# Kernel optimization log

Measured on AMD Instinct MI355X. Metric: run time of the kernel, lower is better.

## Reference

```python
import jax, jax.numpy as jnp
import numpy as np

B, T, C = 4, 2048, 768
N_HEADS = 16
HEAD_DIM = C // N_HEADS  # 48
ROPE_BASE = 10000.0


def setup_inputs() -> dict:
    key = jax.random.key(0)
    ks = jax.random.split(key, 6)
    s = 0.02
    return {
        "hidden_states": jax.random.normal(ks[0], (B, T, C), dtype=jnp.float32),
        "attention_mask": jnp.ones((B, T), dtype=jnp.float32),
        "Wq": jax.random.normal(ks[1], (C, C), dtype=jnp.float32) * s,
        "bq": jnp.zeros((C,), dtype=jnp.float32),
        "Wk": jax.random.normal(ks[2], (C, C), dtype=jnp.float32) * s,
        "bk": jnp.zeros((C,), dtype=jnp.float32),
        "Wv": jax.random.normal(ks[3], (C, C), dtype=jnp.float32) * s,
        "bv": jnp.zeros((C,), dtype=jnp.float32),
        "Wo": jax.random.normal(ks[4], (C, C), dtype=jnp.float32) * s,
        "bo": jnp.zeros((C,), dtype=jnp.float32),
    }


def _rotate_half(x):
    x1, x2 = jnp.split(x, 2, axis=-1)
    return jnp.concatenate([-x2, x1], axis=-1)


def reference(hidden_states, attention_mask, Wq, bq, Wk, bk, Wv, bv, Wo, bo):
    b, t, c = hidden_states.shape
    h, d = N_HEADS, c // N_HEADS

    def split_heads(x):  # [b,t,c] -> [b,h,t,d]
        return x.reshape(b, t, h, d).transpose(0, 2, 1, 3)

    q = split_heads(hidden_states @ Wq.T + bq)
    k = split_heads(hidden_states @ Wk.T + bk)
    v = split_heads(hidden_states @ Wv.T + bv)

    # rotary embedding: cos/sin [t, d]
    pos = jnp.arange(t, dtype=jnp.float32)
    inv_freq = 1.0 / (ROPE_BASE ** (jnp.arange(0, d, 2, dtype=jnp.float32) / d))
    freqs = pos[:, None] * inv_freq[None, :]          # [t, d/2]
    emb = jnp.concatenate([freqs, freqs], axis=-1)    # [t, d]
    cos, sin = jnp.cos(emb), jnp.sin(emb)
    q = q * cos + _rotate_half(q) * sin
    k = k * cos + _rotate_half(k) * sin

    scores = jnp.einsum('bhqd,bhkd->bhqk', q, k) / jnp.sqrt(jnp.asarray(d, q.dtype))
    # additive padding mask: (1 - mask) * -10000, broadcast [b,1,1,t]
    scores = scores + (1.0 - attention_mask)[:, None, None, :] * -10000.0
    # causal mask with -inf
    causal = jnp.tril(jnp.ones((t, t), dtype=bool))
    scores = jnp.where(causal[None, None], scores, -jnp.inf)

    probs = jax.nn.softmax(scores, axis=-1)
    ctx = jnp.einsum('bhqk,bhkd->bhqd', probs, v)
    ctx = ctx.transpose(0, 2, 1, 3).reshape(b, t, c)
    return ctx @ Wo.T + bo
```

## Files before the change

kernel.cpp:

```cpp
#include <hip/hip_runtime.h>
#include <hip/hip_bf16.h>
#include <math.h>

#define BB 4
#define TT 2048
#define CC 768
#define NHD 16
#define HD 48
#define NQT 32

typedef __hip_bfloat16 bf16;
typedef __attribute__((ext_vector_type(8))) short short8;
typedef __attribute__((ext_vector_type(4))) float floatx4;

__device__ __forceinline__ unsigned short f2bf(float x) {
    bf16 h = __float2bfloat16(x);
    return *(unsigned short*)&h;
}
__device__ __forceinline__ float bfu2f(unsigned short u) {
    return __uint_as_float(((unsigned)u) << 16);
}

__device__ __forceinline__ void gl_lds16(const void* g, void* s) {
    __builtin_amdgcn_global_load_lds((const __attribute__((address_space(1))) void*)g,
                                     (__attribute__((address_space(3))) void*)s, 16, 0, 0);
}

__global__ __launch_bounds__(256) void cast_hs(const float* __restrict__ src,
                                               unsigned short* __restrict__ dst) {
    int i = (blockIdx.x * 256 + threadIdx.x) * 4;
    float4 v = *(const float4*)(src + i);
    ushort4 p;
    p.x = f2bf(v.x); p.y = f2bf(v.y); p.z = f2bf(v.z); p.w = f2bf(v.w);
    *(ushort4*)(dst + i) = p;
}

__global__ __launch_bounds__(256) void cast_w4(const float* __restrict__ s0, const float* __restrict__ s1,
                                               const float* __restrict__ s2, const float* __restrict__ s3,
                                               unsigned short* __restrict__ d0, unsigned short* __restrict__ d1,
                                               unsigned short* __restrict__ d2, unsigned short* __restrict__ d3) {
    const float* s; unsigned short* d;
    switch (blockIdx.y) {
        case 0: s = s0; d = d0; break;
        case 1: s = s1; d = d1; break;
        case 2: s = s2; d = d2; break;
        default: s = s3; d = d3; break;
    }
    int i = (blockIdx.x * 256 + threadIdx.x) * 4;
    float4 v = *(const float4*)(s + i);
    ushort4 p;
    p.x = f2bf(v.x); p.y = f2bf(v.y); p.z = f2bf(v.z); p.w = f2bf(v.w);
    *(ushort4*)(d + i) = p;
}

template <int MODE>
__global__ __launch_bounds__(256) void gemm_mfma(const unsigned short* __restrict__ A,
                                                 const unsigned short* __restrict__ Bw,
                                                 const float* __restrict__ b0p,
                                                 const float* __restrict__ b1p,
                                                 const float* __restrict__ b2p,
                                                 void* __restrict__ out0,
                                                 void* __restrict__ out1,
                                                 void* __restrict__ out2) {
    __shared__ __align__(16) unsigned short As[128][32];
    __shared__ __align__(16) unsigned short Bs[128][32];
    const int tid = threadIdx.x;
    const int w = tid >> 6, lane = tid & 63;
    const int quad = lane >> 4, ln = lane & 15;
    const int wr = w >> 1, wc = w & 1;
    const int n0 = blockIdx.x * 128;
    const int m0 = blockIdx.y * 128;

    const int srow = lane >> 2, sseg = lane & 3;
    const unsigned short* agp0 = A + (size_t)(m0 + w * 16 + srow) * CC + sseg * 8;
    const unsigned short* agp1 = A + (size_t)(m0 + 64 + w * 16 + srow) * CC + sseg * 8;
    const unsigned short* bgp0 = Bw + (size_t)(n0 + w * 16 + srow) * CC + sseg * 8;
    const unsigned short* bgp1 = Bw + (size_t)(n0 + 64 + w * 16 + srow) * CC + sseg * 8;
    void* asl0 = &As[w * 16][0];
    void* asl1 = &As[64 + w * 16][0];
    void* bsl0 = &Bs[w * 16][0];
    void* bsl1 = &Bs[64 + w * 16][0];

    floatx4 acc[4][4];
#pragma unroll
    for (int mi = 0; mi < 4; ++mi)
#pragma unroll
        for (int ni = 0; ni < 4; ++ni) acc[mi][ni] = (floatx4){0.f, 0.f, 0.f, 0.f};

    for (int k0 = 0; k0 < CC; k0 += 32) {
        __syncthreads();
        gl_lds16(agp0 + k0, asl0);
        gl_lds16(agp1 + k0, asl1);
        gl_lds16(bgp0 + k0, bsl0);
        gl_lds16(bgp1 + k0, bsl1);
        __syncthreads();
        short8 af[4], bfr[4];
#pragma unroll
        for (int mi = 0; mi < 4; ++mi) af[mi] = *(const short8*)&As[wr * 64 + mi * 16 + ln][quad * 8];
#pragma unroll
        for (int ni = 0; ni < 4; ++ni) bfr[ni] = *(const short8*)&Bs[wc * 64 + ni * 16 + ln][quad * 8];
#pragma unroll
        for (int mi = 0; mi < 4; ++mi)
#pragma unroll
            for (int ni = 0; ni < 4; ++ni)
                acc[mi][ni] = __builtin_amdgcn_mfma_f32_16x16x32_bf16(af[mi], bfr[ni], acc[mi][ni], 0, 0, 0);
    }

    if (MODE == 0) {
        float* outf = (float*)out0;
        float bv[4];
#pragma unroll
        for (int ni = 0; ni < 4; ++ni) bv[ni] = b0p[n0 + wc * 64 + ni * 16 + ln];
#pragma unroll
        for (int mi = 0; mi < 4; ++mi)
#pragma unroll
            for (int r = 0; r < 4; ++r) {
                size_t row = m0 + wr * 64 + mi * 16 + quad * 4 + r;
#pragma unroll
                for (int ni = 0; ni < 4; ++ni)
                    outf[row * CC + n0 + wc * 64 + ni * 16 + ln] = acc[mi][ni][r] + bv[ni];
            }
    } else {
        const int seg = n0 / CC;
        const int nl0 = n0 - seg * CC;
        const float* bp = (seg == 0) ? b0p : (seg == 1) ? b1p : b2p;
        float bv[4];
#pragma unroll
        for (int ni = 0; ni < 4; ++ni) bv[ni] = bp[nl0 + wc * 64 + ni * 16 + ln];

        if (seg < 2) {
            unsigned short* outb = (unsigned short*)(seg == 0 ? out0 : out1);
#pragma unroll
            for (int mi = 0; mi < 4; ++mi)
#pragma unroll
                for (int r = 0; r < 4; ++r) {
                    size_t row = m0 + wr * 64 + mi * 16 + quad * 4 + r;
#pragma unroll
                    for (int ni = 0; ni < 4; ++ni)
                        outb[row * CC + nl0 + wc * 64 + ni * 16 + ln] = f2bf(acc[mi][ni][r] + bv[ni]);
                }
        } else {
            unsigned short* outb = (unsigned short*)out2;
            const int b = m0 >> 11;
#pragma unroll
            for (int ni = 0; ni < 4; ++ni) {
                int col = nl0 + wc * 64 + ni * 16 + ln;
                int h = col / HD, d = col % HD;
                size_t base = (size_t)((b * NHD + h) * HD + d) * TT;
#pragma unroll
                for (int mi = 0; mi < 4; ++mi) {
                    int t = (m0 & 2047) + wr * 64 + mi * 16 + quad * 4;
                    ushort4 pk;
                    pk.x = f2bf(acc[mi][ni][0] + bv[ni]);
                    pk.y = f2bf(acc[mi][ni][1] + bv[ni]);
                    pk.z = f2bf(acc[mi][ni][2] + bv[ni]);
                    pk.w = f2bf(acc[mi][ni][3] + bv[ni]);
                    *(ushort4*)(outb + base + t) = pk;
                }
            }
        }
    }
}

__global__ __launch_bounds__(256) void rope_bf(unsigned short* __restrict__ q,
                                               unsigned short* __restrict__ k) {
    int idx = blockIdx.x * blockDim.x + threadIdx.x;
    const int HALF = HD / 2;
    int p = idx % HALF;
    int rest = idx / HALF;
    int h = rest % NHD;
    int n = rest / NHD;
    int t = n % TT;
    float inv_freq = powf(10000.0f, -((float)(2 * p) / (float)HD));
    float ang = (float)t * inv_freq;
    float sn, cs;
    sincosf(ang, &sn, &cs);
    size_t base = (size_t)n * CC + h * HD + p;
    float x1 = bfu2f(q[base]), x2 = bfu2f(q[base + HALF]);
    q[base] = f2bf(x1 * cs - x2 * sn);
    q[base + HALF] = f2bf(x2 * cs + x1 * sn);
    x1 = bfu2f(k[base]); x2 = bfu2f(k[base + HALF]);
    k[base] = f2bf(x1 * cs - x2 * sn);
    k[base + HALF] = f2bf(x2 * cs + x1 * sn);
}

__global__ __launch_bounds__(256) void attn_kernel(const unsigned short* __restrict__ qb,
                                                   const unsigned short* __restrict__ kb,
                                                   const unsigned short* __restrict__ vt,
                                                   const float* __restrict__ amask,
                                                   unsigned short* __restrict__ ctx) {
    const int pair = blockIdx.x, h = blockIdx.y, b = blockIdx.z;
    const int tid = threadIdx.x;
    const int w = tid >> 6, lane = tid & 63;
    const int g = lane >> 4, ln = lane & 15;

    __shared__ __align__(16) unsigned short Qs[64][72];
    __shared__ __align__(16) unsigned short Ks[64][72];
    __shared__ __align__(16) unsigned short Vs[48][72];
    __shared__ __align__(16) unsigned short Pw[4][16][72];
    __shared__ __align__(16) float Mb[64];
    __shared__ __align__(16) float alpha_s[4][16];
    __shared__ __align__(16) float l_s[4][16];

    {
        short8 z8 = {0, 0, 0, 0, 0, 0, 0, 0};
        if (tid < 128) {
            *(short8*)&Qs[tid >> 1][48 + (tid & 1) * 8] = z8;
        } else {
            int t2 = tid - 128;
            *(short8*)&Ks[t2 >> 1][48 + (t2 & 1) * 8] = z8;
        }
    }

    const int ck1 = tid + 256;
    const int rK0 = tid / 6, sK0 = tid % 6;
    const int rK1 = ck1 / 6, sK1 = ck1 % 6;
    const int rV0 = tid >> 3, sV0 = tid & 7;
    const int rV1 = ck1 >> 3, sV1 = ck1 & 7;
    const unsigned short* kbase0 = kb + (size_t)(b * TT + rK0) * CC + h * HD + sK0 * 8;
    const unsigned short* kbase1 = kb + (size_t)(b * TT + rK1) * CC + h * HD + sK1 * 8;
    const unsigned short* vbase0 = vt + (size_t)((b * NHD + h) * HD + rV0) * TT + sV0 * 8;
    const unsigned short* vbase1 = vt + (size_t)((b * NHD + h) * HD + rV1) * TT + sV1 * 8;
    const float* mbase = amask + b * TT + (tid & 63);

    const float scale = 0.14433756729740643f;

    for (int rep = 0; rep < 2; ++rep) {
        const int qt = rep ? (NQT - 1 - pair) : pair;
        const int q0 = qt * 64;
        __syncthreads();
        *(short8*)&Qs[rK0][sK0 * 8] =
            *(const short8*)(qb + (size_t)(b * TT + q0 + rK0) * CC + h * HD + sK0 * 8);
        if (tid < 128)
            *(short8*)&Qs[rK1][sK1 * 8] =
                *(const short8*)(qb + (size_t)(b * TT + q0 + rK1) * CC + h * HD + sK1 * 8);

        const unsigned short* kp0 = kbase0;
        const unsigned short* kp1 = kbase1;
        const unsigned short* vp0 = vbase0;
        const unsigned short* vp1 = vbase1;
        const float* mp = mbase;
        short8 kr0, kr1, vr0, vr1;
        float mr = 1.0f;
        kr0 = *(const short8*)kp0;
        vr0 = *(const short8*)vp0;
        if (tid < 128) { kr1 = *(const short8*)kp1; vr1 = *(const short8*)vp1; }
        if (tid < 64) mr = *mp;
        __syncthreads();

        short8 aq0 = *(const short8*)&Qs[w * 16 + ln][g * 8];
        short8 aq1 = *(const short8*)&Qs[w * 16 + ln][32 + g * 8];
        const int q_lane = q0 + w * 16 + ln;

        float m_i = -1e30f, l_i = 0.f;
        floatx4 o0 = {0.f, 0.f, 0.f, 0.f}, o1 = o0, o2 = o0;

        for (int kt = 0; kt <= qt; ++kt) {
            __syncthreads();
            *(short8*)&Ks[rK0][sK0 * 8] = kr0;
            *(short8*)&Vs[rV0][sV0 * 8] = vr0;
            if (tid < 128) {
                *(short8*)&Ks[rK1][sK1 * 8] = kr1;
                *(short8*)&Vs[rV1][sV1 * 8] = vr1;
            }
            if (tid < 64) Mb[tid] = (1.0f - mr) * -10000.0f;
            __syncthreads();

            if (kt < qt) {
                kp0 += (size_t)64 * CC; kr0 = *(const short8*)kp0;
                vp0 += 64;              vr0 = *(const short8*)vp0;
                if (tid < 128) {
                    kp1 += (size_t)64 * CC; kr1 = *(const short8*)kp1;
                    vp1 += 64;              vr1 = *(const short8*)vp1;
                }
                if (tid < 64) { mp += 64; mr = *mp; }
            }

            const int k0 = kt * 64;
            floatx4 sc[4];
#pragma unroll
            for (int c = 0; c < 4; ++c) {
                short8 kf0 = *(const short8*)&Ks[c * 16 + ln][g * 8];
                short8 kf1 = *(const short8*)&Ks[c * 16 + ln][32 + g * 8];
                floatx4 z = {0.f, 0.f, 0.f, 0.f};
                z = __builtin_amdgcn_mfma_f32_16x16x32_bf16(kf0, aq0, z, 0, 0, 0);
                z = __builtin_amdgcn_mfma_f32_16x16x32_bf16(kf1, aq1, z, 0, 0, 0);
                sc[c] = z;
            }

            const bool diag = (kt == qt);
            float p[4][4];
            float mloc = -1e30f;
#pragma unroll
            for (int c = 0; c < 4; ++c) {
                floatx4 mb4 = *(const floatx4*)&Mb[c * 16 + g * 4];
#pragma unroll
                for (int r = 0; r < 4; ++r) {
                    float s = sc[c][r] * scale + mb4[r];
                    if (diag && (k0 + c * 16 + g * 4 + r > q_lane)) s = -1e30f;
                    p[c][r] = s;
                    mloc = fmaxf(mloc, s);
                }
            }
            mloc = fmaxf(mloc, __shfl_xor(mloc, 16));
            mloc = fmaxf(mloc, __shfl_xor(mloc, 32));
            float mnew = fmaxf(m_i, mloc);
            float alpha = __expf(m_i - mnew);
            float rs = 0.f;
#pragma unroll
            for (int c = 0; c < 4; ++c)
#pragma unroll
                for (int r = 0; r < 4; ++r) {
                    float pv = __expf(p[c][r] - mnew);
                    p[c][r] = pv;
                    rs += pv;
                }
            rs += __shfl_xor(rs, 16);
            rs += __shfl_xor(rs, 32);
            m_i = mnew;
            l_i = l_i * alpha + rs;

            if (g == 0) alpha_s[w][ln] = alpha;
            floatx4 a4 = *(const floatx4*)&alpha_s[w][g * 4];
#pragma unroll
            for (int r = 0; r < 4; ++r) { o0[r] *= a4[r]; o1[r] *= a4[r]; o2[r] *= a4[r]; }

#pragma unroll
            for (int c = 0; c < 4; ++c) {
                ushort4 pk;
                pk.x = f2bf(p[c][0]); pk.y = f2bf(p[c][1]);
                pk.z = f2bf(p[c][2]); pk.w = f2bf(p[c][3]);
                *(ushort4*)&Pw[w][ln][c * 16 + g * 4] = pk;
            }
            short8 pa0 = *(const short8*)&Pw[w][ln][g * 8];
            short8 pa1 = *(const short8*)&Pw[w][ln][32 + g * 8];
#pragma unroll
            for (int n = 0; n < 3; ++n) {
                short8 vb0 = *(const short8*)&Vs[n * 16 + ln][g * 8];
                short8 vb1 = *(const short8*)&Vs[n * 16 + ln][32 + g * 8];
                floatx4 acc = (n == 0) ? o0 : (n == 1) ? o1 : o2;
                acc = __builtin_amdgcn_mfma_f32_16x16x32_bf16(pa0, vb0, acc, 0, 0, 0);
                acc = __builtin_amdgcn_mfma_f32_16x16x32_bf16(pa1, vb1, acc, 0, 0, 0);
                if (n == 0) o0 = acc; else if (n == 1) o1 = acc; else o2 = acc;
            }
        }

        if (g == 0) l_s[w][ln] = l_i;
        floatx4 l4 = *(const floatx4*)&l_s[w][g * 4];
#pragma unroll
        for (int r = 0; r < 4; ++r) {
            float inv_l = 1.0f / l4[r];
            int t = q0 + w * 16 + g * 4 + r;
            unsigned short* dst = ctx + (size_t)(b * TT + t) * CC + h * HD;
            dst[ln] = f2bf(o0[r] * inv_l);
            dst[16 + ln] = f2bf(o1[r] * inv_l);
            dst[32 + ln] = f2bf(o2[r] * inv_l);
        }
    }
}

extern "C" void kernel_launch(void* const* d_in, const int* in_sizes, int n_in,
                              void* d_out, int out_size, void* d_ws, size_t ws_size,
                              hipStream_t stream) {
    const float* hs = (const float*)d_in[0];
    const float* amask = (const float*)d_in[1];
    const float* Wq = (const float*)d_in[2];
    const float* bq = (const float*)d_in[3];
    const float* Wk = (const float*)d_in[4];
    const float* bk = (const float*)d_in[5];
    const float* Wv = (const float*)d_in[6];
    const float* bv = (const float*)d_in[7];
    const float* Wo = (const float*)d_in[8];
    const float* bo = (const float*)d_in[9];

    const size_t NELEM = (size_t)BB * TT * CC;
    const size_t WELEM = (size_t)CC * CC;
    unsigned short* hb  = (unsigned short*)d_ws;
    unsigned short* qbuf = hb + NELEM;
    unsigned short* kbuf = qbuf + NELEM;
    unsigned short* vtb = kbuf + NELEM;
    unsigned short* ctxb = vtb + NELEM;
    unsigned short* wqb = ctxb + NELEM;
    unsigned short* wkb = wqb + WELEM;
    unsigned short* wvb = wkb + WELEM;
    unsigned short* wob = wvb + WELEM;

    cast_hs<<<NELEM / 1024, 256, 0, stream>>>(hs, hb);
    dim3 wgrid(WELEM / 1024, 4);
    cast_w4<<<wgrid, 256, 0, stream>>>(Wq, Wk, Wv, Wo, wqb, wkb, wvb, wob);

    dim3 qkvgrid(3 * CC / 128, (BB * TT) / 128);
    gemm_mfma<1><<<qkvgrid, 256, 0, stream>>>(hb, wqb, bq, bk, bv, qbuf, kbuf, vtb);

    int rope_total = BB * TT * NHD * (HD / 2);
    rope_bf<<<rope_total / 256, 256, 0, stream>>>(qbuf, kbuf);

    dim3 agrid(NQT / 2, NHD, BB);
    attn_kernel<<<agrid, 256, 0, stream>>>(qbuf, kbuf, vtb, amask, ctxb);

    dim3 ogrid(CC / 128, (BB * TT) / 128);
    gemm_mfma<0><<<ogrid, 256, 0, stream>>>(ctxb, wob, bo, nullptr, nullptr,
                                            (float*)d_out, nullptr, nullptr);
}
```

Baseline: 271.5 us.

## Widen GEMM K-tile with swizzled LDS, fold softmax scale and mask into QK MFMA

The projection GEMM now stages 64-wide K tiles with an XOR-swizzled shared-memory layout, halving the number of barrier pairs and avoiding LDS bank conflicts. The softmax scale and log2(e) are folded into Q during RoPE. The padding mask bias is stored as an extra K column, matched by a 1.0 in Q's padding lane, so the MFMA adds it directly. Softmax switches to exp2, and probabilities are packed to bf16 with a cheap round-half-up bit trick instead of the full conversion. This trades a small precision change (bf16-rounded mask bias and Q scale, non-RNE rounding) for fewer ALU ops in the attention inner loop.

```diff
diff --git a/kernel.cpp b/kernel.cpp
--- a/kernel.cpp
+++ b/kernel.cpp
@@ -24,6 +24,12 @@
 __device__ __forceinline__ void gl_lds16(const void* g, void* s) {
     __builtin_amdgcn_global_load_lds((const __attribute__((address_space(1))) void*)g,
                                      (__attribute__((address_space(3))) void*)s, 16, 0, 0);
+}
+
+__device__ __forceinline__ unsigned int pk_bf2(float a, float b) {
+    unsigned int ua = __float_as_uint(a) + 0x8000u;
+    unsigned int ub = __float_as_uint(b) + 0x8000u;
+    return __builtin_amdgcn_perm(ub, ua, 0x07060302);
 }
 
 __global__ __launch_bounds__(256) void cast_hs(const float* __restrict__ src,
@@ -62,8 +68,8 @@
                                                  void* __restrict__ out0,
                                                  void* __restrict__ out1,
                                                  void* __restrict__ out2) {
-    __shared__ __align__(16) unsigned short As[128][32];
-    __shared__ __align__(16) unsigned short Bs[128][32];
+    __shared__ __align__(16) unsigned short As[128][64];
+    __shared__ __align__(16) unsigned short Bs[128][64];
     const int tid = threadIdx.x;
     const int w = tid >> 6, lane = tid & 63;
     const int quad = lane >> 4, ln = lane & 15;
@@ -71,15 +77,20 @@
     const int n0 = blockIdx.x * 128;
     const int m0 = blockIdx.y * 128;
 
-    const int srow = lane >> 2, sseg = lane & 3;
-    const unsigned short* agp0 = A + (size_t)(m0 + w * 16 + srow) * CC + sseg * 8;
-    const unsigned short* agp1 = A + (size_t)(m0 + 64 + w * 16 + srow) * CC + sseg * 8;
-    const unsigned short* bgp0 = Bw + (size_t)(n0 + w * 16 + srow) * CC + sseg * 8;
-    const unsigned short* bgp1 = Bw + (size_t)(n0 + 64 + w * 16 + srow) * CC + sseg * 8;
-    void* asl0 = &As[w * 16][0];
-    void* asl1 = &As[64 + w * 16][0];
-    void* bsl0 = &Bs[w * 16][0];
-    void* bsl1 = &Bs[64 + w * 16][0];
+    const int srow = lane >> 3;
+    const int ssw = ((lane & 7) ^ srow) * 8;
+    const unsigned short* agp[4];
+    const unsigned short* bgp[4];
+    void* asl[4];
+    void* bsl[4];
+#pragma unroll
+    for (int i = 0; i < 4; ++i) {
+        const int R = i * 32 + w * 8;
+        agp[i] = A + (size_t)(m0 + R + srow) * CC + ssw;
+        bgp[i] = Bw + (size_t)(n0 + R + srow) * CC + ssw;
+        asl[i] = &As[R][0];
+        bsl[i] = &Bs[R][0];
+    }
 
     floatx4 acc[4][4];
 #pragma unroll
@@ -87,23 +98,32 @@
 #pragma unroll
         for (int ni = 0; ni < 4; ++ni) acc[mi][ni] = (floatx4){0.f, 0.f, 0.f, 0.f};
 
-    for (int k0 = 0; k0 < CC; k0 += 32) {
+    const int ps0 = (quad ^ (ln & 7)) * 8;
+
+    for (int k0 = 0; k0 < CC; k0 += 64) {
         __syncthreads();
-        gl_lds16(agp0 + k0, asl0);
-        gl_lds16(agp1 + k0, asl1);
-        gl_lds16(bgp0 + k0, bsl0);
-        gl_lds16(bgp1 + k0, bsl1);
+#pragma unroll
+        for (int i = 0; i < 4; ++i) {
+            gl_lds16(agp[i] + k0, asl[i]);
+            gl_lds16(bgp[i] + k0, bsl[i]);
+        }
         __syncthreads();
-        short8 af[4], bfr[4];
-#pragma unroll
-        for (int mi = 0; mi < 4; ++mi) af[mi] = *(const short8*)&As[wr * 64 + mi * 16 + ln][quad * 8];
-#pragma unroll
-        for (int ni = 0; ni < 4; ++ni) bfr[ni] = *(const short8*)&Bs[wc * 64 + ni * 16 + ln][quad * 8];
-#pragma unroll
-        for (int mi = 0; mi < 4; ++mi)
+#pragma unroll
+        for (int kh = 0; kh < 2; ++kh) {
+            const int ps = ps0 ^ (kh * 32);
+            short8 af[4], bfr[4];
+#pragma unroll
+            for (int mi = 0; mi < 4; ++mi)
+                af[mi] = *(const short8*)&As[wr * 64 + mi * 16 + ln][ps];
 #pragma unroll
             for (int ni = 0; ni < 4; ++ni)
-                acc[mi][ni] = __builtin_amdgcn_mfma_f32_16x16x32_bf16(af[mi], bfr[ni], acc[mi][ni], 0, 0, 0);
+                bfr[ni] = *(const short8*)&Bs[wc * 64 + ni * 16 + ln][ps];
+#pragma unroll
+            for (int mi = 0; mi < 4; ++mi)
+#pragma unroll
+                for (int ni = 0; ni < 4; ++ni)
+                    acc[mi][ni] = __builtin_amdgcn_mfma_f32_16x16x32_bf16(af[mi], bfr[ni], acc[mi][ni], 0, 0, 0);
+        }
     }
 
     if (MODE == 0) {
@@ -171,14 +191,15 @@
     int h = rest % NHD;
     int n = rest / NHD;
     int t = n % TT;
+    const float QSC = 0.14433756729740643f * 1.4426950408889634f;
     float inv_freq = powf(10000.0f, -((float)(2 * p) / (float)HD));
     float ang = (float)t * inv_freq;
     float sn, cs;
     sincosf(ang, &sn, &cs);
     size_t base = (size_t)n * CC + h * HD + p;
     float x1 = bfu2f(q[base]), x2 = bfu2f(q[base + HALF]);
-    q[base] = f2bf(x1 * cs - x2 * sn);
-    q[base + HALF] = f2bf(x2 * cs + x1 * sn);
+    q[base] = f2bf((x1 * cs - x2 * sn) * QSC);
+    q[base + HALF] = f2bf((x2 * cs + x1 * sn) * QSC);
     x1 = bfu2f(k[base]); x2 = bfu2f(k[base + HALF]);
     k[base] = f2bf(x1 * cs - x2 * sn);
     k[base + HALF] = f2bf(x2 * cs + x1 * sn);
@@ -198,14 +219,15 @@
     __shared__ __align__(16) unsigned short Ks[64][72];
     __shared__ __align__(16) unsigned short Vs[48][72];
     __shared__ __align__(16) unsigned short Pw[4][16][72];
-    __shared__ __align__(16) float Mb[64];
     __shared__ __align__(16) float alpha_s[4][16];
     __shared__ __align__(16) float l_s[4][16];
 
     {
         short8 z8 = {0, 0, 0, 0, 0, 0, 0, 0};
+        short8 o8 = {0x3F80, 0, 0, 0, 0, 0, 0, 0};
         if (tid < 128) {
-            *(short8*)&Qs[tid >> 1][48 + (tid & 1) * 8] = z8;
+            int r = tid >> 1, half = tid & 1;
+            *(short8*)&Qs[r][48 + half * 8] = half ? z8 : o8;
         } else {
             int t2 = tid - 128;
             *(short8*)&Ks[t2 >> 1][48 + (t2 & 1) * 8] = z8;
@@ -222,8 +244,7 @@
     const unsigned short* vbase0 = vt + (size_t)((b * NHD + h) * HD + rV0) * TT + sV0 * 8;
     const unsigned short* vbase1 = vt + (size_t)((b * NHD + h) * HD + rV1) * TT + sV1 * 8;
     const float* mbase = amask + b * TT + (tid & 63);
-
-    const float scale = 0.14433756729740643f;
+    const float MBS = -10000.0f * 1.4426950408889634f;
 
     for (int rep = 0; rep < 2; ++rep) {
         const int qt = rep ? (NQT - 1 - pair) : pair;
@@ -263,7 +284,7 @@
                 *(short8*)&Ks[rK1][sK1 * 8] = kr1;
                 *(short8*)&Vs[rV1][sV1 * 8] = vr1;
             }
-            if (tid < 64) Mb[tid] = (1.0f - mr) * -10000.0f;
+            if (tid < 64) Ks[tid][48] = f2bf((1.0f - mr) * MBS);
             __syncthreads();
 
             if (kt < qt) {
@@ -292,26 +313,24 @@
             float p[4][4];
             float mloc = -1e30f;
 #pragma unroll
-            for (int c = 0; c < 4; ++c) {
-                floatx4 mb4 = *(const floatx4*)&Mb[c * 16 + g * 4];
+            for (int c = 0; c < 4; ++c)
 #pragma unroll
                 for (int r = 0; r < 4; ++r) {
-                    float s = sc[c][r] * scale + mb4[r];
+                    float s = sc[c][r];
                     if (diag && (k0 + c * 16 + g * 4 + r > q_lane)) s = -1e30f;
                     p[c][r] = s;
                     mloc = fmaxf(mloc, s);
                 }
-            }
             mloc = fmaxf(mloc, __shfl_xor(mloc, 16));
             mloc = fmaxf(mloc, __shfl_xor(mloc, 32));
             float mnew = fmaxf(m_i, mloc);
-            float alpha = __expf(m_i - mnew);
+            float alpha = __builtin_amdgcn_exp2f(m_i - mnew);
             float rs = 0.f;
 #pragma unroll
             for (int c = 0; c < 4; ++c)
 #pragma unroll
                 for (int r = 0; r < 4; ++r) {
-                    float pv = __expf(p[c][r] - mnew);
+                    float pv = __builtin_amdgcn_exp2f(p[c][r] - mnew);
                     p[c][r] = pv;
                     rs += pv;
                 }
@@ -327,10 +346,10 @@
 
 #pragma unroll
             for (int c = 0; c < 4; ++c) {
-                ushort4 pk;
-                pk.x = f2bf(p[c][0]); pk.y = f2bf(p[c][1]);
-                pk.z = f2bf(p[c][2]); pk.w = f2bf(p[c][3]);
-                *(ushort4*)&Pw[w][ln][c * 16 + g * 4] = pk;
+                uint2 pk;
+                pk.x = pk_bf2(p[c][0], p[c][1]);
+                pk.y = pk_bf2(p[c][2], p[c][3]);
+                *(uint2*)&Pw[w][ln][c * 16 + g * 4] = pk;
             }
             short8 pa0 = *(const short8*)&Pw[w][ln][g * 8];
             short8 pa1 = *(const short8*)&Pw[w][ln][32 + g * 8];
```

After: 259.3 us. 1.05x faster.
